# Kernel tuning notes

Hardware: AMD Instinct MI355X
Metric: run time of the kernel (lower is better)

## Reference

```python
import jax, jax.numpy as jnp
import numpy as np

B, S, D, H = 8, 1024, 1024, 16
DH = D // H  # 64

def setup_inputs() -> dict:
    key = jax.random.key(0)
    k1, k2, k3 = jax.random.split(key, 3)
    x = jax.random.normal(k1, (B, S, D), dtype=jnp.float32)
    mask = jnp.tril(jnp.ones((S, S), dtype=bool))[None, None]  # causal [1,1,S,S]
    W_qkv = jax.random.normal(k2, (D, 3 * D), dtype=jnp.float32) * 0.02
    W_out = jax.random.normal(k3, (D, D), dtype=jnp.float32) * 0.02
    return {"x": x, "mask": mask, "W_qkv": W_qkv, "W_out": W_out}

def reference(x, mask, W_qkv, W_out):
    qkv = jnp.einsum('bnd,de->bne', x, W_qkv)
    q, k, v = jnp.split(qkv, 3, axis=-1)
    # [b, h, n, dh]
    split_heads = lambda t: t.reshape(B, S, H, DH).transpose(0, 2, 1, 3)
    q, k, v = map(split_heads, (q, k, v))
    attn = jnp.einsum('bhnd,bhmd->bhnm', q, k) / jnp.sqrt(jnp.float32(DH))
    attn = jnp.where(mask, attn, 0.7 * jnp.finfo(attn.dtype).min)
    attn = jax.nn.softmax(attn.astype(jnp.float32), axis=-1).astype(x.dtype)
    out = jnp.einsum('bhnm,bhmd->bhnd', attn, v)
    out = out.transpose(0, 2, 1, 3).reshape(B, S, D)
    return jnp.einsum('bnd,de->bne', out, W_out)
```

## Files before the change

kernel.cpp:

```cpp
#include <hip/hip_runtime.h>
#include <stdint.h>

typedef __attribute__((ext_vector_type(8))) short short8;
typedef __attribute__((ext_vector_type(4))) float floatx4;

__device__ __forceinline__ unsigned short f2bf(float f) {
  union { float f; uint32_t u; } v; v.f = f;
  uint32_t u = v.u;
  return (unsigned short)((u + 0x7FFFu + ((u >> 16) & 1u)) >> 16);
}

__device__ __forceinline__ uint32_t fbits(float f) {
  union { float f; uint32_t u; } v; v.f = f; return v.u;
}
__device__ __forceinline__ uint32_t pkbf(float hi, float lo) {
  return __builtin_amdgcn_perm(fbits(hi), fbits(lo), 0x07060302u);
}

__device__ __forceinline__ void gl_lds16(const void* g, void* l) {
  __builtin_amdgcn_global_load_lds((__attribute__((address_space(1))) void*)g,
                                   (__attribute__((address_space(3))) void*)l,
                                   16, 0, 0);
}

__global__ __launch_bounds__(256) void cast_x_kernel(const float* __restrict__ in,
                                                     unsigned short* __restrict__ out,
                                                     int n4) {
  int i = blockIdx.x * 256 + threadIdx.x;
  if (i >= n4) return;
  float4 v = ((const float4*)in)[i];
  ushort4 o;
  o.x = f2bf(v.x); o.y = f2bf(v.y); o.z = f2bf(v.z); o.w = f2bf(v.w);
  ((ushort4*)out)[i] = o;
}

__global__ __launch_bounds__(256) void transpose_cast2_kernel(const float* __restrict__ in0,
                                                              unsigned short* __restrict__ out0,
                                                              const float* __restrict__ in1,
                                                              unsigned short* __restrict__ out1) {
  __shared__ float tile[32][33];
  const int R = 1024;
  int bx = blockIdx.x;
  const float* in; unsigned short* out; int C;
  if (bx < 96) { in = in0; out = out0; C = 3072; }
  else         { in = in1; out = out1; C = 1024; bx -= 96; }
  int c0 = bx * 32, r0 = blockIdx.y * 32;
  int tx = threadIdx.x & 31;
  int ty = threadIdx.x >> 5;
  for (int i = ty; i < 32; i += 8)
    tile[i][tx] = in[(size_t)(r0 + i) * C + c0 + tx];
  __syncthreads();
  for (int i = ty; i < 32; i += 8)
    out[(size_t)(c0 + i) * R + r0 + tx] = f2bf(tile[tx][i]);
}

__global__ __launch_bounds__(256) void gemm_bt_kernel(const unsigned short* __restrict__ A,
                                                      const unsigned short* __restrict__ Bt,
                                                      int N, int mode,
                                                      unsigned short* __restrict__ qo,
                                                      unsigned short* __restrict__ ko,
                                                      unsigned short* __restrict__ vo,
                                                      float* __restrict__ fo) {
  const int Kd = 1024;
  __shared__ union {
    struct { unsigned short A[2][8192]; unsigned short B[2][8192]; } s;
    float cf[16384];
    unsigned short ch[32768];
  } sm;
  const int tid = threadIdx.x;
  const int w = tid >> 6, lane = tid & 63;
  const int quad = lane >> 4, l16 = lane & 15;
  const int l7 = l16 & 7;
  const int wm = w >> 1, wn = w & 1;
  const int m0 = blockIdx.y * 128, n0 = blockIdx.x * 128;
  const int tr = (mode == 0) && (n0 >= 2048);
  const int r8 = lane >> 3, ch = lane & 7;
  const int sw = (ch ^ r8) * 8;

  floatx4 acc[4][4];
#pragma unroll
  for (int i = 0; i < 4; ++i)
#pragma unroll
    for (int j = 0; j < 4; ++j)
      acc[i][j] = (floatx4){0.f, 0.f, 0.f, 0.f};

  auto stage = [&](int it, int buf) {
    const int k0 = it * 64;
#pragma unroll
    for (int i = 0; i < 4; ++i) {
      const int row = i * 32 + w * 8 + r8;
      gl_lds16(A + (size_t)(m0 + row) * Kd + k0 + sw, (char*)&sm.s.A[buf][0] + i * 4096 + w * 1024);
      gl_lds16(Bt + (size_t)(n0 + row) * Kd + k0 + sw, (char*)&sm.s.B[buf][0] + i * 4096 + w * 1024);
    }
  };

  stage(0, 0);
  __syncthreads();

  for (int it = 0; it < 16; ++it) {
    const int buf = it & 1;
    if (it < 15) stage(it + 1, buf ^ 1);
    const char* Ab = (const char*)&sm.s.A[buf][0];
    const char* Bb = (const char*)&sm.s.B[buf][0];
#pragma unroll
    for (int half = 0; half < 2; ++half) {
      short8 af[4], bf[4];
#pragma unroll
      for (int i = 0; i < 4; ++i)
        af[i] = *(const short8*)(Ab + (wm * 64 + i * 16 + l16) * 128 +
                                 (((half << 2) | quad) ^ l7) * 16);
#pragma unroll
      for (int j = 0; j < 4; ++j)
        bf[j] = *(const short8*)(Bb + (wn * 64 + j * 16 + l16) * 128 +
                                 (((half << 2) | quad) ^ l7) * 16);
      if (!tr) {
#pragma unroll
        for (int i = 0; i < 4; ++i)
#pragma unroll
          for (int j = 0; j < 4; ++j)
            acc[i][j] = __builtin_amdgcn_mfma_f32_16x16x32_bf16(af[i], bf[j], acc[i][j], 0, 0, 0);
      } else {
#pragma unroll
        for (int p = 0; p < 4; ++p)
#pragma unroll
          for (int q = 0; q < 4; ++q)
            acc[p][q] = __builtin_amdgcn_mfma_f32_16x16x32_bf16(bf[p], af[q], acc[p][q], 0, 0, 0);
      }
    }
    __syncthreads();
  }

  if (mode == 1) {
    float* Cs = sm.cf;
#pragma unroll
    for (int i = 0; i < 4; ++i)
#pragma unroll
      for (int j = 0; j < 4; ++j)
#pragma unroll
        for (int r = 0; r < 4; ++r)
          Cs[(wm * 64 + i * 16 + quad * 4 + r) * 128 + wn * 64 + j * 16 + l16] = acc[i][j][r];
    __syncthreads();
#pragma unroll
    for (int c = 0; c < 16; ++c) {
      int idx = c * 256 + tid;
      float4 v = ((const float4*)sm.cf)[idx];
      int row = idx >> 5, col = (idx & 31) * 4;
      *(float4*)&fo[(size_t)(m0 + row) * N + n0 + col] = v;
    }
  } else {
    unsigned short* Cs = sm.ch;
    if (!tr) {
#pragma unroll
      for (int i = 0; i < 4; ++i)
#pragma unroll
        for (int j = 0; j < 4; ++j)
#pragma unroll
          for (int r = 0; r < 4; ++r)
            Cs[(wm * 64 + i * 16 + quad * 4 + r) * 128 + wn * 64 + j * 16 + l16] =
                f2bf(acc[i][j][r]);
    } else {
#pragma unroll
      for (int p = 0; p < 4; ++p)
#pragma unroll
        for (int q = 0; q < 4; ++q)
#pragma unroll
          for (int r = 0; r < 4; ++r)
            Cs[(wn * 64 + p * 16 + quad * 4 + r) * 128 + wm * 64 + q * 16 + l16] =
                f2bf(acc[p][q][r]);
    }
    __syncthreads();
    unsigned short* dst0 = (n0 < 1024) ? qo : ko;
#pragma unroll
    for (int c = 0; c < 8; ++c) {
      int idx = c * 256 + tid;
      short8 v = *(const short8*)((const char*)sm.ch + idx * 16);
      int row = idx >> 4, col = (idx & 15) * 8;
      if (!tr) {
        int m = m0 + row, n = n0 + col;
        int h = (n & 1023) >> 6, dh = n & 63;
        int bb = m >> 10, s = m & 1023;
        *(short8*)&dst0[(size_t)(bb * 16 + h) * 65536 + (size_t)s * 64 + dh] = v;
      } else {
        int n = n0 + row, m = m0 + col;
        int h = (n & 1023) >> 6, dh = n & 63;
        int bb = m >> 10, s0 = m & 1023;
        *(short8*)&vo[(size_t)(bb * 16 + h) * 65536 + (size_t)dh * 1024 + s0] = v;
      }
    }
  }
}

__global__ __launch_bounds__(256, 3) void attn_kernel(const unsigned short* __restrict__ Qb,
                                                      const unsigned short* __restrict__ Kb,
                                                      const unsigned short* __restrict__ VbT,
                                                      unsigned short* __restrict__ AOb) {
  __shared__ unsigned short Kt[2][4096];
  __shared__ unsigned short Vt[2][4096];
  const int tid = threadIdx.x;
  const int w = tid >> 6, lane = tid & 63;
  const int quad = lane >> 4, l16 = lane & 15;
  const int l7 = l16 & 7;
  const int id = blockIdx.x;
  const int by = id >> 3;
  const int blk = (id + by + (id >> 8)) & 7;
  const int bb = by >> 4, hh = by & 15;
  const int qbase = blk * 128 + w * 32;
  const unsigned short* Qp = Qb + (size_t)by * 65536;
  const unsigned short* Kp = Kb + (size_t)by * 65536;
  const unsigned short* Vp = VbT + (size_t)by * 65536;

  short8 bq[2][2];
#pragma unroll
  for (int qt = 0; qt < 2; ++qt)
#pragma unroll
    for (int kh = 0; kh < 2; ++kh)
      bq[qt][kh] = *(const short8*)(Qp + (size_t)(qbase + qt * 16 + l16) * 64 + kh * 32 + quad * 8);

  floatx4 o[2][4];
#pragma unroll
  for (int qt = 0; qt < 2; ++qt)
#pragma unroll
    for (int dt = 0; dt < 4; ++dt) o[qt][dt] = (floatx4){0.f, 0.f, 0.f, 0.f};
  floatx4 psum[2];
  psum[0] = (floatx4){0.f, 0.f, 0.f, 0.f};
  psum[1] = (floatx4){0.f, 0.f, 0.f, 0.f};

  const int ntm = 2 * blk + 2;
  const int r8 = lane >> 3, ch = lane & 7;
  const int sw8 = (ch ^ r8) * 8;

  auto stage = [&](int t, int buf) {
    const int n0 = t * 64;
#pragma unroll
    for (int i = 0; i < 2; ++i) {
      const int c = w * 2 + i;
      const int row = c * 8 + r8;
      gl_lds16(Kp + (size_t)(n0 + row) * 64 + sw8, (char*)&Kt[buf][0] + c * 1024);
      gl_lds16(Vp + (size_t)row * 1024 + n0 + sw8, (char*)&Vt[buf][0] + c * 1024);
    }
  };

  stage(0, 0);
  __syncthreads();

  for (int t = 0; t < ntm; ++t) {
    const int buf = t & 1;
    if (t + 1 < ntm) stage(t + 1, buf ^ 1);
    const int n0 = t * 64;
    if (n0 <= qbase + 31) {
      const char* kbase = (const char*)&Kt[buf][0];
      const char* vbase = (const char*)&Vt[buf][0];
      short8 ak[4][2];
#pragma unroll
      for (int kt = 0; kt < 4; ++kt)
#pragma unroll
        for (int kh = 0; kh < 2; ++kh)
          ak[kt][kh] = *(const short8*)(kbase + (kt * 16 + l16) * 128 +
                                        (((kh << 2) | quad) ^ l7) * 16);
      uint32_t pd[2][4][2];
      const bool full = (n0 + 63 <= qbase);
#pragma unroll
      for (int kt = 0; kt < 4; ++kt) {
#pragma unroll
        for (int qt = 0; qt < 2; ++qt) {
          floatx4 s = (floatx4){0.f, 0.f, 0.f, 0.f};
          s = __builtin_amdgcn_mfma_f32_16x16x32_bf16(ak[kt][0], bq[qt][0], s, 0, 0, 0);
          s = __builtin_amdgcn_mfma_f32_16x16x32_bf16(ak[kt][1], bq[qt][1], s, 0, 0, 0);
          float f[4];
          if (full) {
#pragma unroll
            for (int r = 0; r < 4; ++r) {
              f[r] = exp2f(fmaf(s[r], 0.18033688f, -11.5415603f));
              psum[qt][r] += f[r];
            }
          } else {
            const int query = qbase + qt * 16 + l16;
#pragma unroll
            for (int r = 0; r < 4; ++r) {
              const int key = n0 + kt * 16 + quad * 4 + r;
              float e = exp2f(fmaf(s[r], 0.18033688f, -11.5415603f));
              f[r] = (key <= query) ? e : 0.0f;
              psum[qt][r] += f[r];
            }
          }
          pd[qt][kt][0] = pkbf(f[1], f[0]);
          pd[qt][kt][1] = pkbf(f[3], f[2]);
        }
      }
#pragma unroll
      for (int dt = 0; dt < 4; ++dt) {
        const int row128 = (dt * 16 + l16) * 128;
#pragma unroll
        for (int u = 0; u < 2; ++u) {
          union { short8 v8; ushort4 h[2]; } bv;
          bv.h[0] = *(const ushort4*)(vbase + row128 +
                                      (((u << 2) | (quad >> 1)) ^ l7) * 16 + (quad & 1) * 8);
          bv.h[1] = *(const ushort4*)(vbase + row128 +
                                      (((u << 2) | 2 | (quad >> 1)) ^ l7) * 16 + (quad & 1) * 8);
          union { uint32_t d[4]; short8 v; } pa;
#pragma unroll
          for (int qt = 0; qt < 2; ++qt) {
            pa.d[0] = pd[qt][u * 2][0];     pa.d[1] = pd[qt][u * 2][1];
            pa.d[2] = pd[qt][u * 2 + 1][0]; pa.d[3] = pd[qt][u * 2 + 1][1];
            o[qt][dt] = __builtin_amdgcn_mfma_f32_16x16x32_bf16(pa.v, bv.v8, o[qt][dt], 0, 0, 0);
          }
        }
      }
    }
    __syncthreads();
  }

#pragma unroll
  for (int qt = 0; qt < 2; ++qt) {
    float l = psum[qt][0] + psum[qt][1] + psum[qt][2] + psum[qt][3];
    l += __shfl_xor(l, 16);
    l += __shfl_xor(l, 32);
    float inv[4];
#pragma unroll
    for (int r = 0; r < 4; ++r)
      inv[r] = 1.0f / __shfl(l, quad * 4 + r);
#pragma unroll
    for (int dt = 0; dt < 4; ++dt)
#pragma unroll
      for (int r = 0; r < 4; ++r) {
        int row = qbase + qt * 16 + quad * 4 + r;
        AOb[(size_t)(bb * 1024 + row) * 1024 + hh * 64 + dt * 16 + l16] =
            f2bf(o[qt][dt][r] * inv[r]);
      }
  }
}

extern "C" void kernel_launch(void* const* d_in, const int* in_sizes, int n_in,
                              void* d_out, int out_size, void* d_ws, size_t ws_size,
                              hipStream_t stream) {
  const float* x    = (const float*)d_in[0];
  const float* Wqkv = (const float*)d_in[2];
  const float* Wout = (const float*)d_in[3];
  float* out = (float*)d_out;

  unsigned short* xb    = (unsigned short*)d_ws;
  unsigned short* WqkvT = xb    + (size_t)8 * 1024 * 1024;
  unsigned short* WoutT = WqkvT + (size_t)3 * 1024 * 1024;
  unsigned short* Qb    = WoutT + (size_t)1024 * 1024;
  unsigned short* Kb    = Qb    + (size_t)8 * 1024 * 1024;
  unsigned short* VbT   = Kb    + (size_t)8 * 1024 * 1024;
  unsigned short* AOb   = VbT   + (size_t)8 * 1024 * 1024;

  cast_x_kernel<<<8192, 256, 0, stream>>>(x, xb, 2097152);
  transpose_cast2_kernel<<<dim3(128, 32), 256, 0, stream>>>(Wqkv, WqkvT, Wout, WoutT);
  gemm_bt_kernel<<<dim3(24, 64), 256, 0, stream>>>(xb, WqkvT, 3072, 0, Qb, Kb, VbT, nullptr);
  attn_kernel<<<dim3(1024), 256, 0, stream>>>(Qb, Kb, VbT, AOb);
  gemm_bt_kernel<<<dim3(8, 64), 256, 0, stream>>>(AOb, WoutT, 1024, 1, nullptr, nullptr, nullptr, out);
}
```

Before: 233.7 us.

## Pair causal query blocks per attention CTA, fuse prep kernels, swizzle GEMM epilogue

The attention kernel now gives each block two query tiles, one low and its mirror high (p and 7-p). Every block then walks the same number of key tiles, and each staged K/V tile is reused for both query groups. Row sums now come from an MFMA against a ones vector rather than scalar adds and shuffles, and the occupancy hint drops from 3 to 2 blocks to make room for the extra registers. Separately, the x cast and the weight transpose-casts are merged into one launch, and the GEMM epilogue LDS staging gets an XOR swizzle to avoid bank conflicts. The trade-offs are higher register pressure in attention, half as many attention blocks, and row sums now accumulated from bf16-rounded probabilities.

```diff
diff --git a/kernel.cpp b/kernel.cpp
--- a/kernel.cpp
+++ b/kernel.cpp
@@ -23,28 +23,29 @@
                                    16, 0, 0);
 }
 
-__global__ __launch_bounds__(256) void cast_x_kernel(const float* __restrict__ in,
-                                                     unsigned short* __restrict__ out,
-                                                     int n4) {
-  int i = blockIdx.x * 256 + threadIdx.x;
-  if (i >= n4) return;
-  float4 v = ((const float4*)in)[i];
-  ushort4 o;
-  o.x = f2bf(v.x); o.y = f2bf(v.y); o.z = f2bf(v.z); o.w = f2bf(v.w);
-  ((ushort4*)out)[i] = o;
-}
-
-__global__ __launch_bounds__(256) void transpose_cast2_kernel(const float* __restrict__ in0,
-                                                              unsigned short* __restrict__ out0,
-                                                              const float* __restrict__ in1,
-                                                              unsigned short* __restrict__ out1) {
+__global__ __launch_bounds__(256) void prep_kernel(const float* __restrict__ x,
+                                                   unsigned short* __restrict__ xb,
+                                                   const float* __restrict__ Wqkv,
+                                                   unsigned short* __restrict__ WqkvT,
+                                                   const float* __restrict__ Wout,
+                                                   unsigned short* __restrict__ WoutT) {
   __shared__ float tile[32][33];
+  int id = blockIdx.x;
+  if (id < 8192) {
+    int i = id * 256 + threadIdx.x;
+    float4 v = ((const float4*)x)[i];
+    ushort4 o;
+    o.x = f2bf(v.x); o.y = f2bf(v.y); o.z = f2bf(v.z); o.w = f2bf(v.w);
+    ((ushort4*)xb)[i] = o;
+    return;
+  }
+  id -= 8192;
+  int bx = id & 127, r0 = (id >> 7) * 32;
   const int R = 1024;
-  int bx = blockIdx.x;
   const float* in; unsigned short* out; int C;
-  if (bx < 96) { in = in0; out = out0; C = 3072; }
-  else         { in = in1; out = out1; C = 1024; bx -= 96; }
-  int c0 = bx * 32, r0 = blockIdx.y * 32;
+  if (bx < 96) { in = Wqkv; out = WqkvT; C = 3072; }
+  else         { in = Wout; out = WoutT; C = 1024; bx -= 96; }
+  int c0 = bx * 32;
   int tx = threadIdx.x & 31;
   int ty = threadIdx.x >> 5;
   for (int i = ty; i < 32; i += 8)
@@ -137,15 +138,18 @@
 #pragma unroll
       for (int j = 0; j < 4; ++j)
 #pragma unroll
-        for (int r = 0; r < 4; ++r)
-          Cs[(wm * 64 + i * 16 + quad * 4 + r) * 128 + wn * 64 + j * 16 + l16] = acc[i][j][r];
+        for (int r = 0; r < 4; ++r) {
+          int row = wm * 64 + i * 16 + quad * 4 + r;
+          int col = wn * 64 + j * 16 + l16;
+          Cs[row * 128 + (col ^ ((row & 7) << 2))] = acc[i][j][r];
+        }
     __syncthreads();
 #pragma unroll
     for (int c = 0; c < 16; ++c) {
       int idx = c * 256 + tid;
-      float4 v = ((const float4*)sm.cf)[idx];
-      int row = idx >> 5, col = (idx & 31) * 4;
-      *(float4*)&fo[(size_t)(m0 + row) * N + n0 + col] = v;
+      int row = idx >> 5, fc = idx & 31;
+      float4 v = *(const float4*)&sm.cf[row * 128 + ((fc ^ (row & 7)) << 2)];
+      *(float4*)&fo[(size_t)(m0 + row) * N + n0 + fc * 4] = v;
     }
   } else {
     unsigned short* Cs = sm.ch;
@@ -155,26 +159,31 @@
 #pragma unroll
         for (int j = 0; j < 4; ++j)
 #pragma unroll
-          for (int r = 0; r < 4; ++r)
-            Cs[(wm * 64 + i * 16 + quad * 4 + r) * 128 + wn * 64 + j * 16 + l16] =
-                f2bf(acc[i][j][r]);
+          for (int r = 0; r < 4; ++r) {
+            int row = wm * 64 + i * 16 + quad * 4 + r;
+            int col = wn * 64 + j * 16 + l16;
+            Cs[row * 128 + (col ^ ((row & 7) << 3))] = f2bf(acc[i][j][r]);
+          }
     } else {
 #pragma unroll
       for (int p = 0; p < 4; ++p)
 #pragma unroll
         for (int q = 0; q < 4; ++q)
 #pragma unroll
-          for (int r = 0; r < 4; ++r)
-            Cs[(wn * 64 + p * 16 + quad * 4 + r) * 128 + wm * 64 + q * 16 + l16] =
-                f2bf(acc[p][q][r]);
+          for (int r = 0; r < 4; ++r) {
+            int row = wn * 64 + p * 16 + quad * 4 + r;
+            int col = wm * 64 + q * 16 + l16;
+            Cs[row * 128 + (col ^ ((row & 7) << 3))] = f2bf(acc[p][q][r]);
+          }
     }
     __syncthreads();
     unsigned short* dst0 = (n0 < 1024) ? qo : ko;
 #pragma unroll
     for (int c = 0; c < 8; ++c) {
       int idx = c * 256 + tid;
-      short8 v = *(const short8*)((const char*)sm.ch + idx * 16);
-      int row = idx >> 4, col = (idx & 15) * 8;
+      int row = idx >> 4, lc = idx & 15;
+      short8 v = *(const short8*)&sm.ch[row * 128 + ((lc ^ (row & 7)) << 3)];
+      int col = lc * 8;
       if (!tr) {
         int m = m0 + row, n = n0 + col;
         int h = (n & 1023) >> 6, dh = n & 63;
@@ -190,7 +199,7 @@
   }
 }
 
-__global__ __launch_bounds__(256, 3) void attn_kernel(const unsigned short* __restrict__ Qb,
+__global__ __launch_bounds__(256, 2) void attn_kernel(const unsigned short* __restrict__ Qb,
                                                       const unsigned short* __restrict__ Kb,
                                                       const unsigned short* __restrict__ VbT,
                                                       unsigned short* __restrict__ AOb) {
@@ -201,31 +210,41 @@
   const int quad = lane >> 4, l16 = lane & 15;
   const int l7 = l16 & 7;
   const int id = blockIdx.x;
-  const int by = id >> 3;
-  const int blk = (id + by + (id >> 8)) & 7;
+  const int by = id >> 2;
+  const int p = id & 3;
   const int bb = by >> 4, hh = by & 15;
-  const int qbase = blk * 128 + w * 32;
+  const int qlo = p * 128 + w * 32;
+  const int qhi = (7 - p) * 128 + w * 32;
   const unsigned short* Qp = Qb + (size_t)by * 65536;
   const unsigned short* Kp = Kb + (size_t)by * 65536;
   const unsigned short* Vp = VbT + (size_t)by * 65536;
 
-  short8 bq[2][2];
-#pragma unroll
-  for (int qt = 0; qt < 2; ++qt)
-#pragma unroll
-    for (int kh = 0; kh < 2; ++kh)
-      bq[qt][kh] = *(const short8*)(Qp + (size_t)(qbase + qt * 16 + l16) * 64 + kh * 32 + quad * 8);
-
-  floatx4 o[2][4];
-#pragma unroll
-  for (int qt = 0; qt < 2; ++qt)
-#pragma unroll
-    for (int dt = 0; dt < 4; ++dt) o[qt][dt] = (floatx4){0.f, 0.f, 0.f, 0.f};
-  floatx4 psum[2];
-  psum[0] = (floatx4){0.f, 0.f, 0.f, 0.f};
-  psum[1] = (floatx4){0.f, 0.f, 0.f, 0.f};
-
-  const int ntm = 2 * blk + 2;
+  short8 bq[2][2][2];
+#pragma unroll
+  for (int g = 0; g < 2; ++g)
+#pragma unroll
+    for (int qt = 0; qt < 2; ++qt)
+#pragma unroll
+      for (int kh = 0; kh < 2; ++kh)
+        bq[g][qt][kh] = *(const short8*)(Qp + (size_t)((g ? qhi : qlo) + qt * 16 + l16) * 64 +
+                                         kh * 32 + quad * 8);
+
+  floatx4 o[2][2][4];
+  floatx4 ps[2][2];
+#pragma unroll
+  for (int g = 0; g < 2; ++g)
+#pragma unroll
+    for (int qt = 0; qt < 2; ++qt) {
+      ps[g][qt] = (floatx4){0.f, 0.f, 0.f, 0.f};
+#pragma unroll
+      for (int dt = 0; dt < 4; ++dt) o[g][qt][dt] = (floatx4){0.f, 0.f, 0.f, 0.f};
+    }
+
+  short8 ones;
+#pragma unroll
+  for (int i = 0; i < 8; ++i) ones[i] = (short)0x3F80;
+
+  const int T = 16 - 2 * p;
   const int r8 = lane >> 3, ch = lane & 7;
   const int sw8 = (ch ^ r8) * 8;
 
@@ -243,11 +262,12 @@
   stage(0, 0);
   __syncthreads();
 
-  for (int t = 0; t < ntm; ++t) {
+  for (int t = 0; t < T; ++t) {
     const int buf = t & 1;
-    if (t + 1 < ntm) stage(t + 1, buf ^ 1);
+    if (t + 1 < T) stage(t + 1, buf ^ 1);
     const int n0 = t * 64;
-    if (n0 <= qbase + 31) {
+    const bool alo = (n0 <= qlo + 31), ahi = (n0 <= qhi + 31);
+    if (alo | ahi) {
       const char* kbase = (const char*)&Kt[buf][0];
       const char* vbase = (const char*)&Vt[buf][0];
       short8 ak[4][2];
@@ -257,36 +277,44 @@
         for (int kh = 0; kh < 2; ++kh)
           ak[kt][kh] = *(const short8*)(kbase + (kt * 16 + l16) * 128 +
                                         (((kh << 2) | quad) ^ l7) * 16);
-      uint32_t pd[2][4][2];
-      const bool full = (n0 + 63 <= qbase);
-#pragma unroll
-      for (int kt = 0; kt < 4; ++kt) {
-#pragma unroll
-        for (int qt = 0; qt < 2; ++qt) {
-          floatx4 s = (floatx4){0.f, 0.f, 0.f, 0.f};
-          s = __builtin_amdgcn_mfma_f32_16x16x32_bf16(ak[kt][0], bq[qt][0], s, 0, 0, 0);
-          s = __builtin_amdgcn_mfma_f32_16x16x32_bf16(ak[kt][1], bq[qt][1], s, 0, 0, 0);
-          float f[4];
-          if (full) {
-#pragma unroll
-            for (int r = 0; r < 4; ++r) {
-              f[r] = exp2f(fmaf(s[r], 0.18033688f, -11.5415603f));
-              psum[qt][r] += f[r];
+      union PaU { short8 v; uint32_t d[4]; };
+      PaU pa[2][2][2];
+
+      auto score = [&](int g, int qb) {
+        const bool full = (n0 + 63 <= qb);
+#pragma unroll
+        for (int kt = 0; kt < 4; ++kt)
+#pragma unroll
+          for (int qt = 0; qt < 2; ++qt) {
+            floatx4 s = (floatx4){0.f, 0.f, 0.f, 0.f};
+            s = __builtin_amdgcn_mfma_f32_16x16x32_bf16(ak[kt][0], bq[g][qt][0], s, 0, 0, 0);
+            s = __builtin_amdgcn_mfma_f32_16x16x32_bf16(ak[kt][1], bq[g][qt][1], s, 0, 0, 0);
+            float f[4];
+            if (full) {
+#pragma unroll
+              for (int r = 0; r < 4; ++r)
+                f[r] = exp2f(fmaf(s[r], 0.18033688f, -11.5415603f));
+            } else {
+              const int query = qb + qt * 16 + l16;
+#pragma unroll
+              for (int r = 0; r < 4; ++r) {
+                const int key = n0 + kt * 16 + quad * 4 + r;
+                float e = exp2f(fmaf(s[r], 0.18033688f, -11.5415603f));
+                f[r] = (key <= query) ? e : 0.0f;
+              }
             }
-          } else {
-            const int query = qbase + qt * 16 + l16;
-#pragma unroll
-            for (int r = 0; r < 4; ++r) {
-              const int key = n0 + kt * 16 + quad * 4 + r;
-              float e = exp2f(fmaf(s[r], 0.18033688f, -11.5415603f));
-              f[r] = (key <= query) ? e : 0.0f;
-              psum[qt][r] += f[r];
-            }
-          }
-          pd[qt][kt][0] = pkbf(f[1], f[0]);
-          pd[qt][kt][1] = pkbf(f[3], f[2]);
-        }
-      }
+            pa[g][qt][kt >> 1].d[(kt & 1) * 2 + 0] = pkbf(f[1], f[0]);
+            pa[g][qt][kt >> 1].d[(kt & 1) * 2 + 1] = pkbf(f[3], f[2]);
+          }
+#pragma unroll
+        for (int qt = 0; qt < 2; ++qt)
+#pragma unroll
+          for (int u = 0; u < 2; ++u)
+            ps[g][qt] = __builtin_amdgcn_mfma_f32_16x16x32_bf16(pa[g][qt][u].v, ones, ps[g][qt], 0, 0, 0);
+      };
+      if (alo) score(0, qlo);
+      if (ahi) score(1, qhi);
+
 #pragma unroll
       for (int dt = 0; dt < 4; ++dt) {
         const int row128 = (dt * 16 + l16) * 128;
@@ -297,12 +325,15 @@
                                       (((u << 2) | (quad >> 1)) ^ l7) * 16 + (quad & 1) * 8);
           bv.h[1] = *(const ushort4*)(vbase + row128 +
                                       (((u << 2) | 2 | (quad >> 1)) ^ l7) * 16 + (quad & 1) * 8);
-          union { uint32_t d[4]; short8 v; } pa;
-#pragma unroll
-          for (int qt = 0; qt < 2; ++qt) {
-            pa.d[0] = pd[qt][u * 2][0];     pa.d[1] = pd[qt][u * 2][1];
-            pa.d[2] = pd[qt][u * 2 + 1][0]; pa.d[3] = pd[qt][u * 2 + 1][1];
-            o[qt][dt] = __builtin_amdgcn_mfma_f32_16x16x32_bf16(pa.v, bv.v8, o[qt][dt], 0, 0, 0);
+          if (alo) {
+#pragma unroll
+            for (int qt = 0; qt < 2; ++qt)
+              o[0][qt][dt] = __builtin_amdgcn_mfma_f32_16x16x32_bf16(pa[0][qt][u].v, bv.v8, o[0][qt][dt], 0, 0, 0);
+          }
+          if (ahi) {
+#pragma unroll
+            for (int qt = 0; qt < 2; ++qt)
+              o[1][qt][dt] = __builtin_amdgcn_mfma_f32_16x16x32_bf16(pa[1][qt][u].v, bv.v8, o[1][qt][dt], 0, 0, 0);
           }
         }
       }
@@ -311,22 +342,22 @@
   }
 
 #pragma unroll
-  for (int qt = 0; qt < 2; ++qt) {
-    float l = psum[qt][0] + psum[qt][1] + psum[qt][2] + psum[qt][3];
-    l += __shfl_xor(l, 16);
-    l += __shfl_xor(l, 32);
-    float inv[4];
-#pragma unroll
-    for (int r = 0; r < 4; ++r)
-      inv[r] = 1.0f / __shfl(l, quad * 4 + r);
-#pragma unroll
-    for (int dt = 0; dt < 4; ++dt)
-#pragma unroll
-      for (int r = 0; r < 4; ++r) {
-        int row = qbase + qt * 16 + quad * 4 + r;
-        AOb[(size_t)(bb * 1024 + row) * 1024 + hh * 64 + dt * 16 + l16] =
-            f2bf(o[qt][dt][r] * inv[r]);
-      }
+  for (int g = 0; g < 2; ++g) {
+    const int qb = g ? qhi : qlo;
+#pragma unroll
+    for (int qt = 0; qt < 2; ++qt) {
+      float inv[4];
+#pragma unroll
+      for (int r = 0; r < 4; ++r) inv[r] = 1.0f / ps[g][qt][r];
+#pragma unroll
+      for (int dt = 0; dt < 4; ++dt)
+#pragma unroll
+        for (int r = 0; r < 4; ++r) {
+          int row = qb + qt * 16 + quad * 4 + r;
+          AOb[(size_t)(bb * 1024 + row) * 1024 + hh * 64 + dt * 16 + l16] =
+              f2bf(o[g][qt][dt][r] * inv[r]);
+        }
+    }
   }
 }
 
@@ -346,9 +377,8 @@
   unsigned short* VbT   = Kb    + (size_t)8 * 1024 * 1024;
   unsigned short* AOb   = VbT   + (size_t)8 * 1024 * 1024;
 
-  cast_x_kernel<<<8192, 256, 0, stream>>>(x, xb, 2097152);
-  transpose_cast2_kernel<<<dim3(128, 32), 256, 0, stream>>>(Wqkv, WqkvT, Wout, WoutT);
+  prep_kernel<<<12288, 256, 0, stream>>>(x, xb, Wqkv, WqkvT, Wout, WoutT);
   gemm_bt_kernel<<<dim3(24, 64), 256, 0, stream>>>(xb, WqkvT, 3072, 0, Qb, Kb, VbT, nullptr);
-  attn_kernel<<<dim3(1024), 256, 0, stream>>>(Qb, Kb, VbT, AOb);
+  attn_kernel<<<512, 256, 0, stream>>>(Qb, Kb, VbT, AOb);
   gemm_bt_kernel<<<dim3(8, 64), 256, 0, stream>>>(AOb, WoutT, 1024, 1, nullptr, nullptr, nullptr, out);
 }
```

Measured after the change: 226.7 us. -3.0%, faster.
